# Kernel optimization log

Measured on AMD Instinct MI355X. Metric: run time of the kernel, lower is better.

Reference implementation:

```python
import jax, jax.numpy as jnp
import numpy as np

MAX_ABS = 1.0          # assumed get_max_abs('T')
DT = 0.01              # forward default dt
TWO_PI = 2.0 * np.pi
B, D, N = 4096, 2048, 4096


def setup_inputs() -> dict:
    key = jax.random.key(0)
    k0, k1 = jax.random.split(key, 2)
    x = jax.random.normal(k0, (B, D), dtype=jnp.float32)
    # nn.Linear params
    W = jax.random.normal(k1, (N, D), dtype=jnp.float32) * (1.0 / np.sqrt(D))
    b = jnp.zeros((N,), dtype=jnp.float32)
    # oscillator params (as initialized in __init__)
    amplitude = jnp.ones((N,), dtype=jnp.float32)
    frequency = jnp.ones((N,), dtype=jnp.float32)
    phase_offset = jnp.zeros((N,), dtype=jnp.float32)
    damping = jnp.full((N,), 0.01, dtype=jnp.float32)
    return {"x": x, "W": W, "b": b, "amplitude": amplitude,
            "frequency": frequency, "phase_offset": phase_offset,
            "damping": damping}


def reference(x, W, b, amplitude, frequency, phase_offset, damping):
    # driving force: [B, N]
    force = x @ W.T + b
    omega_sq = (TWO_PI * frequency) ** 2  # [N]
    # t starts at 0 and is incremented ONCE per forward call
    t = DT

    def step(carry, f):
        state, vel = carry
        accel = -omega_sq * state - damping * vel + f
        vel = vel + accel * DT
        state = state + vel * DT
        return (state, vel), state

    init = (jnp.zeros((N,), x.dtype), jnp.zeros((N,), x.dtype))
    (_, _), states = jax.lax.scan(step, init, force)  # states: [B, N]

    # sinusoid term is identical for every batch step (t fixed within forward)
    osc = amplitude * jnp.sin(TWO_PI * frequency * t + phase_offset)  # [N]
    out = jnp.clip(states + osc, -MAX_ABS, MAX_ABS)
    return out
```

## Files before the change

kernel.cpp:

```cpp
#include <hip/hip_runtime.h>
#include <hip/hip_bf16.h>
#include <math.h>

#define MDIM 4096
#define KDIM 2048
#define NDIM 4096
#define DT   0.01f
#define TWO_PI_F 6.283185307179586f
#define CH 64
#define CL 64

typedef __attribute__((ext_vector_type(8))) short bf16x8;
typedef __attribute__((ext_vector_type(4))) float f32x4;

__device__ __forceinline__ unsigned short f2bf(float f) {
  unsigned int u = __float_as_uint(f);
  u += 0x7FFFu + ((u >> 16) & 1u);
  return (unsigned short)(u >> 16);
}
__device__ __forceinline__ float bf2f(unsigned short u) {
  return __uint_as_float(((unsigned int)u) << 16);
}

__global__ void cast2_bf16_kernel(const float* __restrict__ s0,
                                  unsigned short* __restrict__ d0,
                                  const float* __restrict__ s1,
                                  unsigned short* __restrict__ d1,
                                  int n4each) {
  int i = blockIdx.x * blockDim.x + threadIdx.x;
  const float4* sp;
  ushort4* dp;
  int j;
  if (i < n4each) { sp = (const float4*)s0; dp = (ushort4*)d0; j = i; }
  else            { sp = (const float4*)s1; dp = (ushort4*)d1; j = i - n4each; }
  float4 v = sp[j];
  ushort4 o;
  o.x = f2bf(v.x); o.y = f2bf(v.y); o.z = f2bf(v.z); o.w = f2bf(v.w);
  dp[j] = o;
}

__global__ __launch_bounds__(256, 2) void gemm_scan_kernel(
    const unsigned short* __restrict__ A,
    const unsigned short* __restrict__ Bm,
    const float* __restrict__ bias,
    const float* __restrict__ freq,
    const float* __restrict__ damp,
    unsigned short* __restrict__ zpart,
    float* __restrict__ chunkS,
    float* __restrict__ chunkV) {
  __shared__ __align__(16) unsigned short smem[16384];
  unsigned short* sA = smem;
  unsigned short* sB = smem + 4096;

  const int tid  = threadIdx.x;
  const int lane = tid & 63;
  const int wave = tid >> 6;
  const int wr = wave >> 1;
  const int wc = wave & 1;
  const int q  = lane >> 4;
  const int lm = lane & 15;

  const int bM = blockIdx.x * 128;
  const int bN = blockIdx.y * 128;

  f32x4 acc[4][4];
#pragma unroll
  for (int i = 0; i < 4; i++)
#pragma unroll
    for (int j = 0; j < 4; j++) acc[i][j] = (f32x4){0.f, 0.f, 0.f, 0.f};

  const int idx0 = tid;
  const int idx1 = tid + 256;
  const int r0 = idx0 >> 2, g0 = idx0 & 3;
  const int r1 = idx1 >> 2, g1 = idx1 & 3;
  const int dst0 = r0 * 32 + ((g0 ^ ((r0 >> 1) & 3)) * 8);
  const int dst1 = r1 * 32 + ((g1 ^ ((r1 >> 1) & 3)) * 8);
  const unsigned short* gA0 = A  + (size_t)(bM + r0) * KDIM + g0 * 8;
  const unsigned short* gA1 = A  + (size_t)(bM + r1) * KDIM + g1 * 8;
  const unsigned short* gB0 = Bm + (size_t)(bN + r0) * KDIM + g0 * 8;
  const unsigned short* gB1 = Bm + (size_t)(bN + r1) * KDIM + g1 * 8;
  const int rq = (q ^ ((lm >> 1) & 3)) * 8;

  for (int k0 = 0; k0 < KDIM; k0 += 32) {
    uint4 av0 = *(const uint4*)(gA0 + k0);
    uint4 av1 = *(const uint4*)(gA1 + k0);
    uint4 bv0 = *(const uint4*)(gB0 + k0);
    uint4 bv1 = *(const uint4*)(gB1 + k0);
    __syncthreads();
    *(uint4*)&sA[dst0] = av0;
    *(uint4*)&sA[dst1] = av1;
    *(uint4*)&sB[dst0] = bv0;
    *(uint4*)&sB[dst1] = bv1;
    __syncthreads();

    bf16x8 af[4], bfr[4];
#pragma unroll
    for (int mt = 0; mt < 4; mt++)
      af[mt]  = *(const bf16x8*)&sA[(wr * 64 + mt * 16 + lm) * 32 + rq];
#pragma unroll
    for (int nt = 0; nt < 4; nt++)
      bfr[nt] = *(const bf16x8*)&sB[(wc * 64 + nt * 16 + lm) * 32 + rq];

#pragma unroll
    for (int mt = 0; mt < 4; mt++)
#pragma unroll
      for (int nt = 0; nt < 4; nt++)
        acc[mt][nt] = __builtin_amdgcn_mfma_f32_16x16x32_bf16(
            af[mt], bfr[nt], acc[mt][nt], 0, 0, 0);
  }

  __syncthreads();
  unsigned short* sT = smem + wave * 4096;
#pragma unroll
  for (int nt = 0; nt < 4; nt++) {
    const float bz = bias[bN + wc * 64 + nt * 16 + lm];
#pragma unroll
    for (int mt = 0; mt < 4; mt++)
#pragma unroll
      for (int r = 0; r < 4; r++)
        sT[(mt * 16 + q * 4 + r) * 64 + nt * 16 + lm] =
            f2bf(acc[mt][nt][r] + bz);
  }
  __syncthreads();

  const int gcol = bN + wc * 64 + lane;
  const float om  = TWO_PI_F * freq[gcol];
  const float osq = om * om;
  const float dp  = damp[gcol];
  float s = 0.f, v = 0.f;
#pragma unroll 8
  for (int i = 0; i < CL; i++) {
    float f = bf2f(sT[i * 64 + lane]);
    v += (-osq * s - dp * v + f) * DT;
    s += v * DT;
    sT[i * 64 + lane] = f2bf(s);
  }
  const int chunk = 2 * blockIdx.x + wr;
  chunkS[chunk * NDIM + gcol] = s;
  chunkV[chunk * NDIM + gcol] = v;
  __syncthreads();

#pragma unroll
  for (int k = 0; k < 8; k++) {
    int slot = lane + 64 * k;
    int row  = slot >> 3;
    int col8 = (slot & 7) * 8;
    *(uint4*)&zpart[(size_t)(bM + wr * 64 + row) * NDIM + bN + wc * 64 + col8] =
        *(uint4*)&sT[row * 64 + col8];
  }
}

__global__ void scan_pass2_inplace(float* __restrict__ chunkS,
                                   float* __restrict__ chunkV,
                                   const float* __restrict__ freq,
                                   const float* __restrict__ damp) {
  int n = blockIdx.x * blockDim.x + threadIdx.x;
  float om = TWO_PI_F * freq[n];
  float osq = om * om;
  float dp = damp[n];
  float a00 = 1.f - osq * DT * DT, a01 = DT * (1.f - dp * DT);
  float a10 = -osq * DT,           a11 = 1.f - dp * DT;
#pragma unroll
  for (int i = 0; i < 6; i++) {
    float b00 = a00 * a00 + a01 * a10;
    float b01 = a00 * a01 + a01 * a11;
    float b10 = a10 * a00 + a11 * a10;
    float b11 = a10 * a01 + a11 * a11;
    a00 = b00; a01 = b01; a10 = b10; a11 = b11;
  }
  float cs = 0.f, cv = 0.f;
#pragma unroll 8
  for (int c = 0; c < CH; c++) {
    float ls = chunkS[c * NDIM + n];
    float lv = chunkV[c * NDIM + n];
    chunkS[c * NDIM + n] = cs;
    chunkV[c * NDIM + n] = cv;
    float ns = a00 * cs + a01 * cv + ls;
    float nv = a10 * cs + a11 * cv + lv;
    cs = ns; cv = nv;
  }
}

__global__ void scan_out_carry(const unsigned short* __restrict__ zpart,
                               const float* __restrict__ amp,
                               const float* __restrict__ freq,
                               const float* __restrict__ phase,
                               const float* __restrict__ damp,
                               const float* __restrict__ carryS,
                               const float* __restrict__ carryV,
                               float* __restrict__ out) {
  int gid = blockIdx.x * blockDim.x + threadIdx.x;
  int n4 = gid & (NDIM / 4 - 1);
  int c  = gid >> 10;
  int n  = n4 * 4;

  float4 fr = *(const float4*)&freq[n];
  float4 dv = *(const float4*)&damp[n];
  float4 am = *(const float4*)&amp[n];
  float4 ph = *(const float4*)&phase[n];
  float omv[4] = {TWO_PI_F * fr.x, TWO_PI_F * fr.y, TWO_PI_F * fr.z, TWO_PI_F * fr.w};
  float dpv[4] = {dv.x, dv.y, dv.z, dv.w};
  float amv[4] = {am.x, am.y, am.z, am.w};
  float phv[4] = {ph.x, ph.y, ph.z, ph.w};
  float m00[4], m01[4], m10[4], m11[4], osc[4];
#pragma unroll
  for (int j = 0; j < 4; j++) {
    float osq = omv[j] * omv[j];
    m00[j] = 1.f - osq * DT * DT;  m01[j] = DT * (1.f - dpv[j] * DT);
    m10[j] = -osq * DT;            m11[j] = 1.f - dpv[j] * DT;
    osc[j] = amv[j] * sinf(omv[j] * DT + phv[j]);
  }

  float4 csv = *(const float4*)&carryS[c * NDIM + n];
  float4 cvv = *(const float4*)&carryV[c * NDIM + n];
  float hs[4] = {csv.x, csv.y, csv.z, csv.w};
  float hv[4] = {cvv.x, cvv.y, cvv.z, cvv.w};

  const unsigned short* zp = zpart + (size_t)c * CL * NDIM + n;
  float* op = out + (size_t)c * CL * NDIM + n;
#pragma unroll 4
  for (int i = 0; i < CL; i++) {
    ushort4 zv = *(const ushort4*)&zp[(size_t)i * NDIM];
    float z[4] = {bf2f(zv.x), bf2f(zv.y), bf2f(zv.z), bf2f(zv.w)};
    float o[4];
#pragma unroll
    for (int j = 0; j < 4; j++) {
      float t = m00[j] * hs[j] + m01[j] * hv[j];
      float u = m10[j] * hs[j] + m11[j] * hv[j];
      hs[j] = t; hv[j] = u;
      o[j] = fminf(1.f, fmaxf(-1.f, hs[j] + z[j] + osc[j]));
    }
    *(float4*)&op[(size_t)i * NDIM] = (float4){o[0], o[1], o[2], o[3]};
  }
}

__global__ __launch_bounds__(256, 2) void gemm_bt_kernel(
    const unsigned short* __restrict__ A,
    const unsigned short* __restrict__ Bm,
    const float* __restrict__ bias,
    unsigned short* __restrict__ C) {
  __shared__ __align__(16) unsigned short sA[128 * 32];
  __shared__ __align__(16) unsigned short sB[128 * 32];

  const int tid  = threadIdx.x;
  const int lane = tid & 63;
  const int wave = tid >> 6;
  const int wr = wave >> 1;
  const int wc = wave & 1;
  const int q  = lane >> 4;
  const int lm = lane & 15;

  const int bM = blockIdx.x * 128;
  const int bN = blockIdx.y * 128;

  f32x4 acc[4][4];
#pragma unroll
  for (int i = 0; i < 4; i++)
#pragma unroll
    for (int j = 0; j < 4; j++) acc[i][j] = (f32x4){0.f, 0.f, 0.f, 0.f};

  const int idx0 = tid;
  const int idx1 = tid + 256;
  const int r0 = idx0 >> 2, g0 = idx0 & 3;
  const int r1 = idx1 >> 2, g1 = idx1 & 3;
  const int dst0 = r0 * 32 + ((g0 ^ ((r0 >> 1) & 3)) * 8);
  const int dst1 = r1 * 32 + ((g1 ^ ((r1 >> 1) & 3)) * 8);
  const unsigned short* gA0 = A  + (size_t)(bM + r0) * KDIM + g0 * 8;
  const unsigned short* gA1 = A  + (size_t)(bM + r1) * KDIM + g1 * 8;
  const unsigned short* gB0 = Bm + (size_t)(bN + r0) * KDIM + g0 * 8;
  const unsigned short* gB1 = Bm + (size_t)(bN + r1) * KDIM + g1 * 8;
  const int rq = (q ^ ((lm >> 1) & 3)) * 8;

  for (int k0 = 0; k0 < KDIM; k0 += 32) {
    uint4 av0 = *(const uint4*)(gA0 + k0);
    uint4 av1 = *(const uint4*)(gA1 + k0);
    uint4 bv0 = *(const uint4*)(gB0 + k0);
    uint4 bv1 = *(const uint4*)(gB1 + k0);
    __syncthreads();
    *(uint4*)&sA[dst0] = av0;
    *(uint4*)&sA[dst1] = av1;
    *(uint4*)&sB[dst0] = bv0;
    *(uint4*)&sB[dst1] = bv1;
    __syncthreads();

    bf16x8 af[4], bfr[4];
#pragma unroll
    for (int mt = 0; mt < 4; mt++)
      af[mt]  = *(const bf16x8*)&sA[(wr * 64 + mt * 16 + lm) * 32 + rq];
#pragma unroll
    for (int nt = 0; nt < 4; nt++)
      bfr[nt] = *(const bf16x8*)&sB[(wc * 64 + nt * 16 + lm) * 32 + rq];

#pragma unroll
    for (int mt = 0; mt < 4; mt++)
#pragma unroll
      for (int nt = 0; nt < 4; nt++)
        acc[mt][nt] = __builtin_amdgcn_mfma_f32_16x16x32_bf16(
            af[mt], bfr[nt], acc[mt][nt], 0, 0, 0);
  }

#pragma unroll
  for (int nt = 0; nt < 4; nt++) {
    const int col = bN + wc * 64 + nt * 16 + lm;
    const float bz = bias[col];
#pragma unroll
    for (int mt = 0; mt < 4; mt++) {
      const int row0 = bM + wr * 64 + mt * 16 + q * 4;
#pragma unroll
      for (int r = 0; r < 4; r++)
        C[(size_t)(row0 + r) * NDIM + col] = f2bf(acc[mt][nt][r] + bz);
    }
  }
}

__global__ void scan_pass1(const unsigned short* __restrict__ force,
                           const float* __restrict__ freq,
                           const float* __restrict__ damp,
                           float* __restrict__ chunkS,
                           float* __restrict__ chunkV) {
  int gid = blockIdx.x * blockDim.x + threadIdx.x;
  int n4 = gid & (NDIM / 4 - 1);
  int c  = gid >> 10;
  int n  = n4 * 4;
  float4 fr = *(const float4*)&freq[n];
  float4 dv = *(const float4*)&damp[n];
  float osq[4] = {TWO_PI_F * fr.x, TWO_PI_F * fr.y, TWO_PI_F * fr.z, TWO_PI_F * fr.w};
  float dp[4]  = {dv.x, dv.y, dv.z, dv.w};
  float s[4] = {0.f, 0.f, 0.f, 0.f}, v[4] = {0.f, 0.f, 0.f, 0.f};
#pragma unroll
  for (int j = 0; j < 4; j++) osq[j] *= osq[j];
  const unsigned short* fp = force + (size_t)c * CL * NDIM + n;
#pragma unroll 4
  for (int i = 0; i < CL; i++) {
    ushort4 fv = *(const ushort4*)&fp[(size_t)i * NDIM];
    float f[4] = {bf2f(fv.x), bf2f(fv.y), bf2f(fv.z), bf2f(fv.w)};
#pragma unroll
    for (int j = 0; j < 4; j++) {
      float a = -osq[j] * s[j] - dp[j] * v[j] + f[j];
      v[j] += a * DT;
      s[j] += v[j] * DT;
    }
  }
  *(float4*)&chunkS[c * NDIM + n] = (float4){s[0], s[1], s[2], s[3]};
  *(float4*)&chunkV[c * NDIM + n] = (float4){v[0], v[1], v[2], v[3]};
}

__global__ void scan_pass2(const float* __restrict__ chunkS,
                           const float* __restrict__ chunkV,
                           const float* __restrict__ freq,
                           const float* __restrict__ damp,
                           float* __restrict__ carryS,
                           float* __restrict__ carryV) {
  int n = blockIdx.x * blockDim.x + threadIdx.x;
  float om = TWO_PI_F * freq[n];
  float osq = om * om;
  float dp = damp[n];
  float a00 = 1.f - osq * DT * DT, a01 = DT * (1.f - dp * DT);
  float a10 = -osq * DT,           a11 = 1.f - dp * DT;
#pragma unroll
  for (int i = 0; i < 6; i++) {
    float b00 = a00 * a00 + a01 * a10;
    float b01 = a00 * a01 + a01 * a11;
    float b10 = a10 * a00 + a11 * a10;
    float b11 = a10 * a01 + a11 * a11;
    a00 = b00; a01 = b01; a10 = b10; a11 = b11;
  }
  float cs = 0.f, cv = 0.f;
#pragma unroll 8
  for (int c = 0; c < CH; c++) {
    carryS[c * NDIM + n] = cs;
    carryV[c * NDIM + n] = cv;
    float ls = chunkS[c * NDIM + n];
    float lv = chunkV[c * NDIM + n];
    float ns = a00 * cs + a01 * cv + ls;
    float nv = a10 * cs + a11 * cv + lv;
    cs = ns; cv = nv;
  }
}

__global__ void scan_pass3(const unsigned short* __restrict__ force,
                           const float* __restrict__ amp,
                           const float* __restrict__ freq,
                           const float* __restrict__ phase,
                           const float* __restrict__ damp,
                           const float* __restrict__ carryS,
                           const float* __restrict__ carryV,
                           float* __restrict__ out) {
  int gid = blockIdx.x * blockDim.x + threadIdx.x;
  int n4 = gid & (NDIM / 4 - 1);
  int c  = gid >> 10;
  int n  = n4 * 4;
  float4 fr = *(const float4*)&freq[n];
  float4 dv = *(const float4*)&damp[n];
  float4 am = *(const float4*)&amp[n];
  float4 ph = *(const float4*)&phase[n];
  float om[4] = {TWO_PI_F * fr.x, TWO_PI_F * fr.y, TWO_PI_F * fr.z, TWO_PI_F * fr.w};
  float dp[4] = {dv.x, dv.y, dv.z, dv.w};
  float osq[4], osc[4], s[4], v[4];
  float amv[4] = {am.x, am.y, am.z, am.w};
  float phv[4] = {ph.x, ph.y, ph.z, ph.w};
#pragma unroll
  for (int j = 0; j < 4; j++) {
    osq[j] = om[j] * om[j];
    osc[j] = amv[j] * sinf(om[j] * DT + phv[j]);
  }
  float4 csv = *(const float4*)&carryS[c * NDIM + n];
  float4 cvv = *(const float4*)&carryV[c * NDIM + n];
  s[0] = csv.x; s[1] = csv.y; s[2] = csv.z; s[3] = csv.w;
  v[0] = cvv.x; v[1] = cvv.y; v[2] = cvv.z; v[3] = cvv.w;
  const unsigned short* fp = force + (size_t)c * CL * NDIM + n;
  float* op = out + (size_t)c * CL * NDIM + n;
#pragma unroll 4
  for (int i = 0; i < CL; i++) {
    ushort4 fv = *(const ushort4*)&fp[(size_t)i * NDIM];
    float f[4] = {bf2f(fv.x), bf2f(fv.y), bf2f(fv.z), bf2f(fv.w)};
    float o[4];
#pragma unroll
    for (int j = 0; j < 4; j++) {
      float a = -osq[j] * s[j] - dp[j] * v[j] + f[j];
      v[j] += a * DT;
      s[j] += v[j] * DT;
      o[j] = fminf(1.f, fmaxf(-1.f, s[j] + osc[j]));
    }
    *(float4*)&op[(size_t)i * NDIM] = (float4){o[0], o[1], o[2], o[3]};
  }
}

extern "C" void kernel_launch(void* const* d_in, const int* in_sizes, int n_in,
                              void* d_out, int out_size, void* d_ws, size_t ws_size,
                              hipStream_t stream) {
  const float* x     = (const float*)d_in[0];
  const float* W     = (const float*)d_in[1];
  const float* bias  = (const float*)d_in[2];
  const float* amp   = (const float*)d_in[3];
  const float* freq  = (const float*)d_in[4];
  const float* phase = (const float*)d_in[5];
  const float* damp  = (const float*)d_in[6];

  const size_t MiB = 1024 * 1024;
  const int n4each = MDIM * KDIM / 4;
  dim3 gg(MDIM / 128, NDIM / 128);

  if (ws_size >= 66 * MiB) {
    unsigned short* xbf   = (unsigned short*)d_ws;
    unsigned short* wbf   = xbf + (size_t)MDIM * KDIM;
    unsigned short* zpart = wbf + (size_t)NDIM * KDIM;
    float* chunkS = (float*)((char*)d_ws + 64 * MiB);
    float* chunkV = chunkS + CH * NDIM;

    cast2_bf16_kernel<<<(2 * n4each + 255) / 256, 256, 0, stream>>>(
        x, xbf, W, wbf, n4each);
    gemm_scan_kernel<<<gg, 256, 0, stream>>>(xbf, wbf, bias, freq, damp,
                                             zpart, chunkS, chunkV);
    scan_pass2_inplace<<<NDIM / 256, 256, 0, stream>>>(chunkS, chunkV,
                                                       freq, damp);
    scan_out_carry<<<CH * NDIM / 4 / 256, 256, 0, stream>>>(
        zpart, amp, freq, phase, damp, chunkS, chunkV, (float*)d_out);
  } else {
    unsigned short* xbf   = (unsigned short*)d_ws;
    unsigned short* wbf   = xbf + (size_t)MDIM * KDIM;
    unsigned short* force = wbf + (size_t)NDIM * KDIM;
    float* chunkS = (float*)d_ws;
    float* chunkV = chunkS + CH * NDIM;
    float* carryS = chunkV + CH * NDIM;
    float* carryV = carryS + CH * NDIM;

    cast2_bf16_kernel<<<(2 * n4each + 255) / 256, 256, 0, stream>>>(
        x, xbf, W, wbf, n4each);
    gemm_bt_kernel<<<gg, 256, 0, stream>>>(xbf, wbf, bias, force);
    scan_pass1<<<CH * NDIM / 4 / 256, 256, 0, stream>>>(force, freq, damp,
                                                        chunkS, chunkV);
    scan_pass2<<<NDIM / 256, 256, 0, stream>>>(chunkS, chunkV, freq, damp,
                                               carryS, carryV);
    scan_pass3<<<CH * NDIM / 4 / 256, 256, 0, stream>>>(
        force, amp, freq, phase, damp, carryS, carryV, (float*)d_out);
  }
}
```

Before: 222.8 us.

## Rewrite fused GEMM+scan with 256x256 tiles, direct-to-LDS loads, and split carry pass

Replaces the 128x128 register-staged GEMM with a 256x256-tile, 512-thread kernel. It uses global_load_lds async copies into a double-buffered 128KB LDS pipeline with explicit vmcnt waits, MFMA priority hints, and an XCD-aware block swizzle. The epilogue now scans four 64-row chunks per block using a swizzled LDS layout. The final carry pass splits each 64-row chunk into four 16-row pieces, using matrix powers to derive the starting state, which raises parallelism. Aims to raise data reuse and overlap loads with MFMA, at the cost of higher LDS use, lower occupancy and more fragile hand scheduling.

```diff
diff --git a/kernel.cpp b/kernel.cpp
--- a/kernel.cpp
+++ b/kernel.cpp
@@ -9,6 +9,7 @@
 #define TWO_PI_F 6.283185307179586f
 #define CH 64
 #define CL 64
+#define TILES (KDIM / 64)
 
 typedef __attribute__((ext_vector_type(8))) short bf16x8;
 typedef __attribute__((ext_vector_type(4))) float f32x4;
@@ -39,7 +40,17 @@
   dp[j] = o;
 }
 
-__global__ __launch_bounds__(256, 2) void gemm_scan_kernel(
+
+__device__ __forceinline__ void gload16(const unsigned short* g,
+                                        unsigned short* l) {
+  __builtin_amdgcn_global_load_lds(
+      (const __attribute__((address_space(1))) unsigned int*)g,
+      (__attribute__((address_space(3))) unsigned int*)l, 16, 0, 0);
+}
+
+#define WAITVM(n) asm volatile("s_waitcnt vmcnt(" #n ")" ::: "memory")
+
+__global__ __launch_bounds__(512, 2) void gemm_scan256_kernel(
     const unsigned short* __restrict__ A,
     const unsigned short* __restrict__ Bm,
     const float* __restrict__ bias,
@@ -48,105 +59,153 @@
     unsigned short* __restrict__ zpart,
     float* __restrict__ chunkS,
     float* __restrict__ chunkV) {
-  __shared__ __align__(16) unsigned short smem[16384];
-  unsigned short* sA = smem;
-  unsigned short* sB = smem + 4096;
+  extern __shared__ __align__(16) unsigned short smem[];
 
   const int tid  = threadIdx.x;
   const int lane = tid & 63;
-  const int wave = tid >> 6;
-  const int wr = wave >> 1;
-  const int wc = wave & 1;
-  const int q  = lane >> 4;
-  const int lm = lane & 15;
-
-  const int bM = blockIdx.x * 128;
-  const int bN = blockIdx.y * 128;
-
-  f32x4 acc[4][4];
-#pragma unroll
-  for (int i = 0; i < 4; i++)
+  const int w    = tid >> 6;
+  const int wr   = w >> 2;
+  const int wc   = w & 3;
+  const int q    = lane >> 4;
+  const int lm   = lane & 15;
+
+  const int bid = blockIdx.x;
+  const int wg  = (bid & 7) * 32 + (bid >> 3);
+  const int tm  = wg >> 4;
+  const int tn  = wg & 15;
+  const int bM  = tm * 256;
+  const int bN  = tn * 256;
+
+  const int srow  = w * 16 + (lane >> 2);
+  const int sslot = (lane & 3) ^ ((lane >> 3) & 3);
+  const unsigned short* gA = A  + (size_t)(bM + srow) * KDIM + sslot * 8;
+  const unsigned short* gB = Bm + (size_t)(bN + srow) * KDIM + sslot * 8;
+  const int ldst = w * 512 + lane * 8;
+
+#define SUNIT(mat, u, ks, rh)                                              \
+  gload16((mat ? gB : gA) + (size_t)(rh) * 128 * KDIM + (u) * 64 + (ks) * 32, \
+          smem + ((u) & 1) * 32768 + (mat) * 16384 + (ks) * 8192 +         \
+              (rh) * 4096 + ldst)
+
+  const int flane = (lm >> 1) & 3;
+  const int aoff  = (wr * 128 + lm) * 32 + ((q ^ flane) * 8);
+  const int boff  = 16384 + (wc * 64 + lm) * 32 + ((q ^ flane) * 8);
+
+  f32x4 acc[8][4];
+#pragma unroll
+  for (int i = 0; i < 8; i++)
 #pragma unroll
     for (int j = 0; j < 4; j++) acc[i][j] = (f32x4){0.f, 0.f, 0.f, 0.f};
 
-  const int idx0 = tid;
-  const int idx1 = tid + 256;
-  const int r0 = idx0 >> 2, g0 = idx0 & 3;
-  const int r1 = idx1 >> 2, g1 = idx1 & 3;
-  const int dst0 = r0 * 32 + ((g0 ^ ((r0 >> 1) & 3)) * 8);
-  const int dst1 = r1 * 32 + ((g1 ^ ((r1 >> 1) & 3)) * 8);
-  const unsigned short* gA0 = A  + (size_t)(bM + r0) * KDIM + g0 * 8;
-  const unsigned short* gA1 = A  + (size_t)(bM + r1) * KDIM + g1 * 8;
-  const unsigned short* gB0 = Bm + (size_t)(bN + r0) * KDIM + g0 * 8;
-  const unsigned short* gB1 = Bm + (size_t)(bN + r1) * KDIM + g1 * 8;
-  const int rq = (q ^ ((lm >> 1) & 3)) * 8;
-
-  for (int k0 = 0; k0 < KDIM; k0 += 32) {
-    uint4 av0 = *(const uint4*)(gA0 + k0);
-    uint4 av1 = *(const uint4*)(gA1 + k0);
-    uint4 bv0 = *(const uint4*)(gB0 + k0);
-    uint4 bv1 = *(const uint4*)(gB1 + k0);
-    __syncthreads();
-    *(uint4*)&sA[dst0] = av0;
-    *(uint4*)&sA[dst1] = av1;
-    *(uint4*)&sB[dst0] = bv0;
-    *(uint4*)&sB[dst1] = bv1;
-    __syncthreads();
-
-    bf16x8 af[4], bfr[4];
-#pragma unroll
-    for (int mt = 0; mt < 4; mt++)
-      af[mt]  = *(const bf16x8*)&sA[(wr * 64 + mt * 16 + lm) * 32 + rq];
-#pragma unroll
-    for (int nt = 0; nt < 4; nt++)
-      bfr[nt] = *(const bf16x8*)&sB[(wc * 64 + nt * 16 + lm) * 32 + rq];
-
-#pragma unroll
-    for (int mt = 0; mt < 4; mt++)
-#pragma unroll
-      for (int nt = 0; nt < 4; nt++)
-        acc[mt][nt] = __builtin_amdgcn_mfma_f32_16x16x32_bf16(
-            af[mt], bfr[nt], acc[mt][nt], 0, 0, 0);
-  }
+  SUNIT(1, 0, 0, 0); SUNIT(1, 0, 0, 1);
+  SUNIT(0, 0, 0, 0); SUNIT(0, 0, 0, 1);
+  SUNIT(1, 0, 1, 0); SUNIT(1, 0, 1, 1);
+  SUNIT(0, 0, 1, 0); SUNIT(0, 0, 1, 1);
+  SUNIT(1, 1, 0, 0); SUNIT(1, 1, 0, 1);
+  SUNIT(0, 1, 0, 0); SUNIT(0, 1, 0, 1);
+  SUNIT(1, 1, 1, 0); SUNIT(1, 1, 1, 1);
+
+#define LDA(KS, MH)                                                        \
+  _Pragma("unroll") for (int m = 0; m < 4; ++m) af[m] =                    \
+      *(const bf16x8*)&smem[bufo + (KS) + (MH) + aoff + m * 512]
+#define LDB(KS)                                                            \
+  _Pragma("unroll") for (int n = 0; n < 4; ++n) bfv[n] =                   \
+      *(const bf16x8*)&smem[bufo + (KS) + boff + n * 512]
+#define MFMA16(MB)                                                         \
+  __builtin_amdgcn_s_setprio(1);                                           \
+  _Pragma("unroll") for (int m = 0; m < 4; ++m)                            \
+      _Pragma("unroll") for (int n = 0; n < 4; ++n)                        \
+          acc[(MB) + m][n] = __builtin_amdgcn_mfma_f32_16x16x32_bf16(      \
+              af[m], bfv[n], acc[(MB) + m][n], 0, 0, 0);                   \
+  __builtin_amdgcn_s_setprio(0)
+
+#pragma unroll 2
+  for (int t = 0; t < TILES; ++t) {
+    const int bufo = (t & 1) * 32768;
+    bf16x8 af[4], bfv[4];
+
+    if (t < TILES - 1) WAITVM(10); else WAITVM(4);
+    __builtin_amdgcn_s_barrier();
+    LDA(0, 0);
+    LDB(0);
+    if (t + 1 < TILES) { SUNIT(0, t + 1, 1, 0); SUNIT(0, t + 1, 1, 1); }
+    MFMA16(0);
+
+    __builtin_amdgcn_s_barrier();
+    LDA(0, 2048);
+    if (t + 2 < TILES) { SUNIT(1, t + 2, 0, 0); SUNIT(1, t + 2, 0, 1); }
+    MFMA16(4);
+
+    if (t < TILES - 2) WAITVM(10);
+    else if (t == TILES - 2) WAITVM(8);
+    else WAITVM(0);
+    __builtin_amdgcn_s_barrier();
+    LDA(8192, 0);
+    LDB(8192);
+    if (t + 2 < TILES) { SUNIT(0, t + 2, 0, 0); SUNIT(0, t + 2, 0, 1); }
+    MFMA16(0);
+
+    __builtin_amdgcn_s_barrier();
+    LDA(8192, 2048);
+    if (t + 2 < TILES) { SUNIT(1, t + 2, 1, 0); SUNIT(1, t + 2, 1, 1); }
+    MFMA16(4);
+  }
+#undef LDA
+#undef LDB
+#undef MFMA16
+#undef SUNIT
 
   __syncthreads();
-  unsigned short* sT = smem + wave * 4096;
-#pragma unroll
-  for (int nt = 0; nt < 4; nt++) {
-    const float bz = bias[bN + wc * 64 + nt * 16 + lm];
-#pragma unroll
-    for (int mt = 0; mt < 4; mt++)
-#pragma unroll
-      for (int r = 0; r < 4; r++)
-        sT[(mt * 16 + q * 4 + r) * 64 + nt * 16 + lm] =
-            f2bf(acc[mt][nt][r] + bz);
+
+#pragma unroll
+  for (int n = 0; n < 4; ++n) {
+    const float bz = bias[bN + wc * 64 + n * 16 + lm];
+#pragma unroll
+    for (int M = 0; M < 8; ++M)
+#pragma unroll
+      for (int rr = 0; rr < 4; ++rr) {
+        const int row = wr * 128 + M * 16 + q * 4 + rr;
+        const int col = wc * 64 + ((n ^ q) * 16) + lm;
+        smem[row * 256 + col] = f2bf(acc[M][n][rr] + bz);
+      }
   }
   __syncthreads();
 
-  const int gcol = bN + wc * 64 + lane;
-  const float om  = TWO_PI_F * freq[gcol];
-  const float osq = om * om;
-  const float dp  = damp[gcol];
-  float s = 0.f, v = 0.f;
+  {
+    const int col  = tid & 255;
+    const int ch0  = (tid >> 8) * 2;
+    const int gcol = bN + col;
+    const float om  = TWO_PI_F * freq[gcol];
+    const float osq = om * om;
+    const float dp  = damp[gcol];
+#pragma unroll
+    for (int cc = 0; cc < 2; ++cc) {
+      const int ch = ch0 + cc;
+      float s = 0.f, v = 0.f;
 #pragma unroll 8
-  for (int i = 0; i < CL; i++) {
-    float f = bf2f(sT[i * 64 + lane]);
-    v += (-osq * s - dp * v + f) * DT;
-    s += v * DT;
-    sT[i * 64 + lane] = f2bf(s);
-  }
-  const int chunk = 2 * blockIdx.x + wr;
-  chunkS[chunk * NDIM + gcol] = s;
-  chunkV[chunk * NDIM + gcol] = v;
+      for (int i = 0; i < CL; ++i) {
+        const int row = ch * 64 + i;
+        const int idx = row * 256 + (col ^ (((i >> 2) & 3) << 4));
+        float f = bf2f(smem[idx]);
+        v += (-osq * s - dp * v + f) * DT;
+        s += v * DT;
+        smem[idx] = f2bf(s);
+      }
+      const int chunk = tm * 4 + ch;
+      chunkS[chunk * NDIM + gcol] = s;
+      chunkV[chunk * NDIM + gcol] = v;
+    }
+  }
   __syncthreads();
 
 #pragma unroll
-  for (int k = 0; k < 8; k++) {
-    int slot = lane + 64 * k;
-    int row  = slot >> 3;
-    int col8 = (slot & 7) * 8;
-    *(uint4*)&zpart[(size_t)(bM + wr * 64 + row) * NDIM + bN + wc * 64 + col8] =
-        *(uint4*)&sT[row * 64 + col8];
+  for (int k = 0; k < 16; ++k) {
+    const int slot = tid + 512 * k;
+    const int row  = slot >> 5;
+    const int grp  = slot & 31;
+    const int sgrp = grp ^ (((row >> 2) & 3) << 1);
+    *(uint4*)&zpart[(size_t)(bM + row) * NDIM + bN + grp * 8] =
+        *(const uint4*)&smem[row * 256 + sgrp * 8];
   }
 }
 
@@ -181,17 +240,19 @@
   }
 }
 
-__global__ void scan_out_carry(const unsigned short* __restrict__ zpart,
-                               const float* __restrict__ amp,
-                               const float* __restrict__ freq,
-                               const float* __restrict__ phase,
-                               const float* __restrict__ damp,
-                               const float* __restrict__ carryS,
-                               const float* __restrict__ carryV,
-                               float* __restrict__ out) {
+__global__ void scan_out_carry4(const unsigned short* __restrict__ zpart,
+                                const float* __restrict__ amp,
+                                const float* __restrict__ freq,
+                                const float* __restrict__ phase,
+                                const float* __restrict__ damp,
+                                const float* __restrict__ carryS,
+                                const float* __restrict__ carryV,
+                                float* __restrict__ out) {
   int gid = blockIdx.x * blockDim.x + threadIdx.x;
   int n4 = gid & (NDIM / 4 - 1);
-  int c  = gid >> 10;
+  int cq = gid >> 10;
+  int c  = cq >> 2;
+  int qq = cq & 3;
   int n  = n4 * 4;
 
   float4 fr = *(const float4*)&freq[n];
@@ -213,13 +274,37 @@
 
   float4 csv = *(const float4*)&carryS[c * NDIM + n];
   float4 cvv = *(const float4*)&carryV[c * NDIM + n];
-  float hs[4] = {csv.x, csv.y, csv.z, csv.w};
-  float hv[4] = {cvv.x, cvv.y, cvv.z, cvv.w};
-
-  const unsigned short* zp = zpart + (size_t)c * CL * NDIM + n;
-  float* op = out + (size_t)c * CL * NDIM + n;
+  float cs[4] = {csv.x, csv.y, csv.z, csv.w};
+  float cv[4] = {cvv.x, cvv.y, cvv.z, cvv.w};
+  float hs[4], hv[4];
+#pragma unroll
+  for (int j = 0; j < 4; j++) {
+    float p00 = m00[j], p01 = m01[j], p10 = m10[j], p11 = m11[j];
+#pragma unroll
+    for (int k = 0; k < 4; k++) {
+      float b00 = p00 * p00 + p01 * p10;
+      float b01 = p00 * p01 + p01 * p11;
+      float b10 = p10 * p00 + p11 * p10;
+      float b11 = p10 * p01 + p11 * p11;
+      p00 = b00; p01 = b01; p10 = b10; p11 = b11;
+    }
+    float j00 = 1.f, j01 = 0.f, j10 = 0.f, j11 = 1.f;
+    for (int k = 0; k < qq; k++) {
+      float b00 = j00 * p00 + j01 * p10;
+      float b01 = j00 * p01 + j01 * p11;
+      float b10 = j10 * p00 + j11 * p10;
+      float b11 = j10 * p01 + j11 * p11;
+      j00 = b00; j01 = b01; j10 = b10; j11 = b11;
+    }
+    hs[j] = j00 * cs[j] + j01 * cv[j];
+    hv[j] = j10 * cs[j] + j11 * cv[j];
+  }
+
+  const size_t r0 = (size_t)c * CL + qq * 16;
+  const unsigned short* zp = zpart + r0 * NDIM + n;
+  float* op = out + r0 * NDIM + n;
 #pragma unroll 4
-  for (int i = 0; i < CL; i++) {
+  for (int i = 0; i < 16; ++i) {
     ushort4 zv = *(const ushort4*)&zp[(size_t)i * NDIM];
     float z[4] = {bf2f(zv.x), bf2f(zv.y), bf2f(zv.z), bf2f(zv.w)};
     float o[4];
@@ -439,7 +524,6 @@
 
   const size_t MiB = 1024 * 1024;
   const int n4each = MDIM * KDIM / 4;
-  dim3 gg(MDIM / 128, NDIM / 128);
 
   if (ws_size >= 66 * MiB) {
     unsigned short* xbf   = (unsigned short*)d_ws;
@@ -448,15 +532,24 @@
     float* chunkS = (float*)((char*)d_ws + 64 * MiB);
     float* chunkV = chunkS + CH * NDIM;
 
+    static bool attr_done = false;
+    if (!attr_done) {
+      (void)hipFuncSetAttribute((const void*)gemm_scan256_kernel,
+                                hipFuncAttributeMaxDynamicSharedMemorySize,
+                                131072);
+      attr_done = true;
+    }
+
     cast2_bf16_kernel<<<(2 * n4each + 255) / 256, 256, 0, stream>>>(
         x, xbf, W, wbf, n4each);
-    gemm_scan_kernel<<<gg, 256, 0, stream>>>(xbf, wbf, bias, freq, damp,
-                                             zpart, chunkS, chunkV);
+    gemm_scan256_kernel<<<dim3(256), dim3(512), 131072, stream>>>(
+        xbf, wbf, bias, freq, damp, zpart, chunkS, chunkV);
     scan_pass2_inplace<<<NDIM / 256, 256, 0, stream>>>(chunkS, chunkV,
                                                        freq, damp);
-    scan_out_carry<<<CH * NDIM / 4 / 256, 256, 0, stream>>>(
+    scan_out_carry4<<<CH * 4 * NDIM / 4 / 256, 256, 0, stream>>>(
         zpart, amp, freq, phase, damp, chunkS, chunkV, (float*)d_out);
   } else {
+    dim3 gg(MDIM / 128, NDIM / 128);
     unsigned short* xbf   = (unsigned short*)d_ws;
     unsigned short* wbf   = xbf + (size_t)MDIM * KDIM;
     unsigned short* force = wbf + (size_t)NDIM * KDIM;
```

Result: faster. 207.5 us (-6.8%).
